# Kernel tuning notes

Hardware: AMD Instinct MI355X
Metric: run time of the kernel (lower is better)

The kernel has to match this reference:

```python
import jax, jax.numpy as jnp
import numpy as np

N_QUBITS = 6
N_LAYERS = 3
B, D_IN, HID, D_OUT = 131072, 32, 16, 1


def _apply_1q(state, gate, q):
    """Apply a 1-qubit gate. state: [B,2,...,2] (qubit q at axis q+1).
    gate: [2,2] (shared) or [B,2,2] (per-sample)."""
    s = jnp.moveaxis(state, q + 1, 1)
    if gate.ndim == 2:
        s = jnp.einsum('ij,bj...->bi...', gate, s)
    else:
        s = jnp.einsum('bij,bj...->bi...', gate, s)
    return jnp.moveaxis(s, 1, q + 1)


def _cnot(state, c, t):
    """CNOT with control c, target t (static wire indices)."""
    idx = (slice(None),) * (c + 1) + (1,)
    sub = state[idx]                      # control axis dropped
    ta = t + 1 if t < c else t            # target axis inside sub
    return state.at[idx].set(jnp.flip(sub, axis=ta))


def _expvals_z(state, n):
    p = state.real ** 2 + state.imag ** 2  # probabilities [B,2,...,2]
    outs = []
    for q in range(n):
        axes = tuple(a for a in range(1, n + 1) if a != q + 1)
        m = p.sum(axes)                    # [B,2]
        outs.append(m[:, 0] - m[:, 1])
    return jnp.stack(outs, axis=-1)        # [B,n]


def quantum_circuit(angles, weights):
    """AngleEmbedding(RY) + BasicEntanglerLayers(RX + CNOT ring), PauliZ expvals."""
    b = angles.shape[0]
    state = jnp.zeros((b,) + (2,) * N_QUBITS, jnp.complex64)
    state = state.at[(slice(None),) + (0,) * N_QUBITS].set(1.0 + 0.0j)
    # per-sample RY embedding
    half = angles * 0.5
    c, s = jnp.cos(half), jnp.sin(half)
    for q in range(N_QUBITS):
        g = jnp.stack([jnp.stack([c[:, q], -s[:, q]], -1),
                       jnp.stack([s[:, q],  c[:, q]], -1)], -2).astype(jnp.complex64)
        state = _apply_1q(state, g, q)
    # entangler layers: RX(w) on each wire, then CNOT ring
    for l in range(N_LAYERS):
        hw = weights[l] * 0.5
        cw = jnp.cos(hw).astype(jnp.complex64)
        sw = (-1j) * jnp.sin(hw).astype(jnp.complex64)
        for q in range(N_QUBITS):
            g = jnp.stack([jnp.stack([cw[q], sw[q]]),
                           jnp.stack([sw[q], cw[q]])])
            state = _apply_1q(state, g, q)
        for q in range(N_QUBITS):
            state = _cnot(state, q, (q + 1) % N_QUBITS)
    return _expvals_z(state, N_QUBITS)


def setup_inputs() -> dict:
    key = jax.random.key(0)
    ks = jax.random.split(key, 11)
    def lin_w(k, fi, fo):
        bnd = 1.0 / np.sqrt(fi)
        return jax.random.uniform(k, (fi, fo), jnp.float32, -bnd, bnd)
    def lin_b(k, fi, fo):
        bnd = 1.0 / np.sqrt(fi)
        return jax.random.uniform(k, (fo,), jnp.float32, -bnd, bnd)
    return {
        'features': jax.random.normal(ks[0], (B, D_IN), jnp.float32),
        'baseline': jax.random.normal(ks[1], (B, D_OUT), jnp.float32),
        'enc_w1': lin_w(ks[2], D_IN, HID), 'enc_b1': lin_b(ks[3], D_IN, HID),
        'enc_w2': lin_w(ks[4], HID, N_QUBITS), 'enc_b2': lin_b(ks[5], HID, N_QUBITS),
        'q_weights': jax.random.uniform(ks[6], (N_LAYERS, N_QUBITS), jnp.float32, 0.0, 2.0 * np.pi),
        'head_w1': lin_w(ks[7], N_QUBITS, HID), 'head_b1': lin_b(ks[8], N_QUBITS, HID),
        'head_w2': lin_w(ks[9], HID, D_OUT), 'head_b2': lin_b(ks[10], HID, D_OUT),
    }


def reference(features, baseline, enc_w1, enc_b1, enc_w2, enc_b2, q_weights,
              head_w1, head_b1, head_w2, head_b2):
    h = jax.nn.gelu(features @ enc_w1 + enc_b1, approximate=False)
    angles = jnp.tanh(h @ enc_w2 + enc_b2)              # [B, n_qubits]
    q_feats = quantum_circuit(angles, q_weights)         # [B, n_qubits]
    r = jax.nn.gelu(q_feats @ head_w1 + head_b1, approximate=False) @ head_w2 + head_b2
    return baseline + r
```

## Files before the change

### kernel.cpp

```cpp
#include <hip/hip_runtime.h>
#include <math.h>


typedef float f32x2 __attribute__((ext_vector_type(2)));

__host__ __device__ constexpr int Lmap(int j) {
    int b5=(j>>5)&1, b4=(j>>4)&1, b3=(j>>3)&1, b2=(j>>2)&1, b1=(j>>1)&1, b0=j&1;
    int o5=b5^b4, o4=b4^b3, o3=b3^b2, o2=b2^b1, o1=b1^b0, o0=b0^b5^b4;
    return (o5<<5)|(o4<<4)|(o3<<3)|(o2<<2)|(o1<<1)|o0;
}
__host__ __device__ constexpr int Linv(int j) {
    int o5=(j>>5)&1, o4=(j>>4)&1, o3=(j>>3)&1, o2=(j>>2)&1, o1=(j>>1)&1, o0=j&1;
    int b4 = o5^o4^o3^o2^o1^o0;
    int b5 = b4^o5;
    int b3 = b4^o4;
    int b2 = b3^o3;
    int b1 = b2^o2;
    int b0 = b1^o1;
    return (b5<<5)|(b4<<4)|(b3<<3)|(b2<<2)|(b1<<1)|b0;
}
__host__ __device__ constexpr int MPc(int q) {
    int m = 1 << (5 - q);
    m = Linv(m); m = Linv(m); m = Linv(m);
    return m;
}
__host__ __device__ constexpr int popc6(int m) {
    int c = 0;
    for (int p = 0; p < 6; ++p) c += (m >> p) & 1;
    return c;
}

__device__ __forceinline__ float fast_tanh(float x) {
    float e = __expf(2.0f * x);
    return 1.0f - 2.0f / (1.0f + e);
}
__device__ __forceinline__ float fast_gelu(float x) {
    float x3 = x * x * x;
    float t  = fast_tanh(fmaf(0.044715f, x3, x) * 0.7978845608028654f);
    return 0.5f * x * (1.0f + t);
}

__global__ void prep_kernel(const float* __restrict__ q_weights,
                            float* __restrict__ Kt)
{
    __shared__ float phi[64];
    const int tid = threadIdx.x;
    {
        int jl = tid;
        float acc = 0.0f;
        for (int l = 0; l < 3; ++l) {
            for (int q = 0; q < 6; ++q)
                acc += q_weights[l * 6 + q] * (((jl >> (5 - q)) & 1) ? 0.5f : -0.5f);
            jl = Lmap(jl);
        }
        phi[tid] = acc;
    }
    __syncthreads();
    if (tid < 48) {
        const int q = tid >> 3, r = tid & 7;
        const int mp = Linv(Linv(Linv(1 << (5 - q))));
        const int F  = (~mp) & 63;
        const int nf = __popc(F), pm = 6 - nf;
        float kv = 0.0f;
        if (r < (1 << nf)) {
            int jb = 0, k = nf;
            for (int p = 5; p >= 0; --p)
                if ((F >> p) & 1) { --k; if ((r >> k) & 1) jb |= 1 << p; }
            float s = 0.0f;
            for (int e = 0; e < (1 << pm); ++e) {
                int je = 0, kk = pm;
                for (int p = 5; p >= 0; --p)
                    if ((mp >> p) & 1) { --kk; if ((e >> kk) & 1) je |= 1 << p; }
                const int j0 = jb | je;
                s += cosf(phi[j0 ^ mp] - phi[j0]);
            }
            kv = s * (1.0f / 64.0f);
        }
        Kt[tid] = kv;
    }
}

template<int Q>
__device__ __forceinline__ float zq_eval(const float (&u2)[6][2], const float (&u01)[6],
                                         const float* __restrict__ K) {
    constexpr int mp = MPc(Q);
    constexpr int F  = (~mp) & 63;
    constexpr int nf = 6 - popc6(mp);
    float cq = 1.0f;
    #pragma unroll
    for (int p = 0; p < 6; ++p) if ((mp >> p) & 1) cq *= u01[p];
    float acc = 0.0f;
    #pragma unroll
    for (int r = 0; r < (1 << nf); ++r) {
        float t = K[Q * 8 + r];
        int k = nf;
        #pragma unroll
        for (int p = 5; p >= 0; --p) if ((F >> p) & 1) { --k; t *= u2[p][(r >> k) & 1]; }
        acc += t;
    }
    return acc * cq;
}

__global__ __launch_bounds__(256) __attribute__((amdgpu_waves_per_eu(2, 2)))
void qrr_kernel(const float* __restrict__ features,
                const float* __restrict__ baseline,
                const float* __restrict__ enc_w1,
                const float* __restrict__ enc_b1,
                const float* __restrict__ enc_w2,
                const float* __restrict__ enc_b2,
                const float* __restrict__ head_w1,
                const float* __restrict__ head_b1,
                const float* __restrict__ head_w2,
                const float* __restrict__ head_b2,
                const float* __restrict__ Kt,
                float* __restrict__ out,
                int n)
{
    const int b = blockIdx.x * 256 + threadIdx.x;
    if (b >= n) return;

    float f[32];
    {
        const float4* fp = reinterpret_cast<const float4*>(features + (size_t)b * 32);
        #pragma unroll
        for (int k = 0; k < 8; ++k) {
            float4 v = fp[k];
            f[4*k+0] = v.x; f[4*k+1] = v.y; f[4*k+2] = v.z; f[4*k+3] = v.w;
        }
    }
    const float base = baseline[b];

    f32x2 h2[8];
    {
        const f32x2* bb = reinterpret_cast<const f32x2*>(enc_b1);
        #pragma unroll
        for (int o = 0; o < 8; ++o) h2[o] = bb[o];
    }
    #pragma unroll
    for (int i = 0; i < 32; ++i) {
        const f32x2 fv = {f[i], f[i]};
        const f32x2* w = reinterpret_cast<const f32x2*>(enc_w1 + i * 16);
        #pragma unroll
        for (int o = 0; o < 8; ++o)
            h2[o] = __builtin_elementwise_fma(fv, w[o], h2[o]);
    }
    float h[16];
    #pragma unroll
    for (int o = 0; o < 8; ++o) {
        h[2*o]   = fast_gelu(h2[o].x);
        h[2*o+1] = fast_gelu(h2[o].y);
    }

    float u2[6][2], u01[6];
    #pragma unroll
    for (int q = 0; q < 6; ++q) {
        float a = enc_b2[q];
        #pragma unroll
        for (int i = 0; i < 16; ++i)
            a = fmaf(h[i], enc_w2[i * 6 + q], a);
        const float half = fast_tanh(a) * 0.5f;
        float s, c;
        __sincosf(half, &s, &c);
        const float e0 = c + s, e1 = c - s;
        const int p = 5 - q;
        u2[p][0] = e0 * e0;
        u2[p][1] = e1 * e1;
        u01[p]   = e0 * e1;
    }

    float z[6];
    z[0] = zq_eval<0>(u2, u01, Kt);
    z[1] = zq_eval<1>(u2, u01, Kt);
    z[2] = zq_eval<2>(u2, u01, Kt);
    z[3] = zq_eval<3>(u2, u01, Kt);
    z[4] = zq_eval<4>(u2, u01, Kt);
    z[5] = zq_eval<5>(u2, u01, Kt);

    f32x2 hh2[8];
    {
        const f32x2* bb = reinterpret_cast<const f32x2*>(head_b1);
        #pragma unroll
        for (int o = 0; o < 8; ++o) hh2[o] = bb[o];
    }
    #pragma unroll
    for (int i = 0; i < 6; ++i) {
        const f32x2 zv = {z[i], z[i]};
        const f32x2* w = reinterpret_cast<const f32x2*>(head_w1 + i * 16);
        #pragma unroll
        for (int o = 0; o < 8; ++o)
            hh2[o] = __builtin_elementwise_fma(zv, w[o], hh2[o]);
    }
    float r = head_b2[0];
    #pragma unroll
    for (int o = 0; o < 8; ++o) {
        r = fmaf(fast_gelu(hh2[o].x), head_w2[2*o],     r);
        r = fmaf(fast_gelu(hh2[o].y), head_w2[2*o + 1], r);
    }

    out[b] = base + r;
}

extern "C" void kernel_launch(void* const* d_in, const int* in_sizes, int n_in,
                              void* d_out, int out_size, void* d_ws, size_t ws_size,
                              hipStream_t stream) {
    const float* features = (const float*)d_in[0];
    const float* baseline = (const float*)d_in[1];
    const float* enc_w1   = (const float*)d_in[2];
    const float* enc_b1   = (const float*)d_in[3];
    const float* enc_w2   = (const float*)d_in[4];
    const float* enc_b2   = (const float*)d_in[5];
    const float* q_weights= (const float*)d_in[6];
    const float* head_w1  = (const float*)d_in[7];
    const float* head_b1  = (const float*)d_in[8];
    const float* head_w2  = (const float*)d_in[9];
    const float* head_b2  = (const float*)d_in[10];
    float* out = (float*)d_out;
    float* Kt  = (float*)d_ws;

    prep_kernel<<<1, 64, 0, stream>>>(q_weights, Kt);

    const int n = in_sizes[0] / 32;
    const int block = 256;
    const int grid = (n + block - 1) / block;
    qrr_kernel<<<grid, block, 0, stream>>>(features, baseline,
                                           enc_w1, enc_b1, enc_w2, enc_b2,
                                           head_w1, head_b1, head_w2, head_b2,
                                           Kt, out, n);
}
```

Measured before the change: 19.28 us.

## Fuse prep kernel into main kernel, recompute K table per block in LDS

Removes the separate single-block prep launch by having every block compute the phi and K tables in shared memory, then copy K into registers. It also simplifies the per-qubit amplitude terms using the identities (c±s)^2 = 1±sin(w) and c^2-s^2 = cos(w), and switches the tanh reciprocal to a hardware rcp intrinsic. The cost is redundant per-block prep work (cosf loops on 48 threads), two block barriers, and 48 extra registers holding K, which may pressure occupancy.

```diff
diff --git a/kernel.cpp b/kernel.cpp
--- a/kernel.cpp
+++ b/kernel.cpp
@@ -30,9 +30,11 @@
     return c;
 }
 
+__device__ __forceinline__ float fast_rcp(float x) { return __builtin_amdgcn_rcpf(x); }
+
 __device__ __forceinline__ float fast_tanh(float x) {
     float e = __expf(2.0f * x);
-    return 1.0f - 2.0f / (1.0f + e);
+    return fmaf(-2.0f, fast_rcp(1.0f + e), 1.0f);
 }
 __device__ __forceinline__ float fast_gelu(float x) {
     float x3 = x * x * x;
@@ -40,12 +42,47 @@
     return 0.5f * x * (1.0f + t);
 }
 
-__global__ void prep_kernel(const float* __restrict__ q_weights,
-                            float* __restrict__ Kt)
+template<int Q>
+__device__ __forceinline__ float zq_eval(const float (&u2)[6][2], const float (&u01)[6],
+                                         const float (&K)[48]) {
+    constexpr int mp = MPc(Q);
+    constexpr int F  = (~mp) & 63;
+    constexpr int nf = 6 - popc6(mp);
+    float cq = 1.0f;
+    #pragma unroll
+    for (int p = 0; p < 6; ++p) if ((mp >> p) & 1) cq *= u01[p];
+    float acc = 0.0f;
+    #pragma unroll
+    for (int r = 0; r < (1 << nf); ++r) {
+        float t = K[Q * 8 + r];
+        int k = nf;
+        #pragma unroll
+        for (int p = 5; p >= 0; --p) if ((F >> p) & 1) { --k; t *= u2[p][(r >> k) & 1]; }
+        acc += t;
+    }
+    return acc * cq;
+}
+
+__global__ __launch_bounds__(256) __attribute__((amdgpu_waves_per_eu(2, 2)))
+void qrr_kernel(const float* __restrict__ features,
+                const float* __restrict__ baseline,
+                const float* __restrict__ enc_w1,
+                const float* __restrict__ enc_b1,
+                const float* __restrict__ enc_w2,
+                const float* __restrict__ enc_b2,
+                const float* __restrict__ q_weights,
+                const float* __restrict__ head_w1,
+                const float* __restrict__ head_b1,
+                const float* __restrict__ head_w2,
+                const float* __restrict__ head_b2,
+                float* __restrict__ out,
+                int n)
 {
     __shared__ float phi[64];
+    __shared__ __align__(16) float KTs[48];
     const int tid = threadIdx.x;
-    {
+
+    if (tid < 64) {
         int jl = tid;
         float acc = 0.0f;
         for (int l = 0; l < 3; ++l) {
@@ -56,6 +93,7 @@
         phi[tid] = acc;
     }
     __syncthreads();
+
     if (tid < 48) {
         const int q = tid >> 3, r = tid & 7;
         const int mp = Linv(Linv(Linv(1 << (5 - q))));
@@ -72,51 +110,25 @@
                 for (int p = 5; p >= 0; --p)
                     if ((mp >> p) & 1) { --kk; if ((e >> kk) & 1) je |= 1 << p; }
                 const int j0 = jb | je;
-                s += cosf(phi[j0 ^ mp] - phi[j0]);
+                s += __cosf(phi[j0 ^ mp] - phi[j0]);
             }
             kv = s * (1.0f / 64.0f);
         }
-        Kt[tid] = kv;
-    }
-}
-
-template<int Q>
-__device__ __forceinline__ float zq_eval(const float (&u2)[6][2], const float (&u01)[6],
-                                         const float* __restrict__ K) {
-    constexpr int mp = MPc(Q);
-    constexpr int F  = (~mp) & 63;
-    constexpr int nf = 6 - popc6(mp);
-    float cq = 1.0f;
-    #pragma unroll
-    for (int p = 0; p < 6; ++p) if ((mp >> p) & 1) cq *= u01[p];
-    float acc = 0.0f;
-    #pragma unroll
-    for (int r = 0; r < (1 << nf); ++r) {
-        float t = K[Q * 8 + r];
-        int k = nf;
-        #pragma unroll
-        for (int p = 5; p >= 0; --p) if ((F >> p) & 1) { --k; t *= u2[p][(r >> k) & 1]; }
-        acc += t;
-    }
-    return acc * cq;
-}
-
-__global__ __launch_bounds__(256) __attribute__((amdgpu_waves_per_eu(2, 2)))
-void qrr_kernel(const float* __restrict__ features,
-                const float* __restrict__ baseline,
-                const float* __restrict__ enc_w1,
-                const float* __restrict__ enc_b1,
-                const float* __restrict__ enc_w2,
-                const float* __restrict__ enc_b2,
-                const float* __restrict__ head_w1,
-                const float* __restrict__ head_b1,
-                const float* __restrict__ head_w2,
-                const float* __restrict__ head_b2,
-                const float* __restrict__ Kt,
-                float* __restrict__ out,
-                int n)
-{
-    const int b = blockIdx.x * 256 + threadIdx.x;
+        KTs[tid] = kv;
+    }
+    __syncthreads();
+
+    float K[48];
+    {
+        const float4* kp = reinterpret_cast<const float4*>(KTs);
+        #pragma unroll
+        for (int i = 0; i < 12; ++i) {
+            float4 v = kp[i];
+            K[4*i+0] = v.x; K[4*i+1] = v.y; K[4*i+2] = v.z; K[4*i+3] = v.w;
+        }
+    }
+
+    const int b = blockIdx.x * 256 + tid;
     if (b >= n) return;
 
     float f[32];
@@ -158,23 +170,22 @@
         #pragma unroll
         for (int i = 0; i < 16; ++i)
             a = fmaf(h[i], enc_w2[i * 6 + q], a);
-        const float half = fast_tanh(a) * 0.5f;
-        float s, c;
-        __sincosf(half, &s, &c);
-        const float e0 = c + s, e1 = c - s;
+        const float w = fast_tanh(a);
+        float sn, cs;
+        __sincosf(w, &sn, &cs);
         const int p = 5 - q;
-        u2[p][0] = e0 * e0;
-        u2[p][1] = e1 * e1;
-        u01[p]   = e0 * e1;
+        u2[p][0] = 1.0f + sn;
+        u2[p][1] = 1.0f - sn;
+        u01[p]   = cs;
     }
 
     float z[6];
-    z[0] = zq_eval<0>(u2, u01, Kt);
-    z[1] = zq_eval<1>(u2, u01, Kt);
-    z[2] = zq_eval<2>(u2, u01, Kt);
-    z[3] = zq_eval<3>(u2, u01, Kt);
-    z[4] = zq_eval<4>(u2, u01, Kt);
-    z[5] = zq_eval<5>(u2, u01, Kt);
+    z[0] = zq_eval<0>(u2, u01, K);
+    z[1] = zq_eval<1>(u2, u01, K);
+    z[2] = zq_eval<2>(u2, u01, K);
+    z[3] = zq_eval<3>(u2, u01, K);
+    z[4] = zq_eval<4>(u2, u01, K);
+    z[5] = zq_eval<5>(u2, u01, K);
 
     f32x2 hh2[8];
     {
@@ -215,15 +226,13 @@
     const float* head_w2  = (const float*)d_in[9];
     const float* head_b2  = (const float*)d_in[10];
     float* out = (float*)d_out;
-    float* Kt  = (float*)d_ws;
-
-    prep_kernel<<<1, 64, 0, stream>>>(q_weights, Kt);
 
     const int n = in_sizes[0] / 32;
     const int block = 256;
     const int grid = (n + block - 1) / block;
     qrr_kernel<<<grid, block, 0, stream>>>(features, baseline,
                                            enc_w1, enc_b1, enc_w2, enc_b2,
+                                           q_weights,
                                            head_w1, head_b1, head_w2, head_b2,
-                                           Kt, out, n);
-}
+                                           out, n);
+}
```

Measured after the change: 15.53 us. -19.4%, faster.
